# Optimization experiments

Measured on AMD Instinct MI355X. Metric: run time of the kernel, lower is better.

## Reference

```python
import jax, jax.numpy as jnp
import numpy as np

H, W, T = 128, 128, 4
BLOCK_W = 16
N = 1024
CHOL_BOUND = jnp.array([0.5, 0.0, 0.0, 0.5, 0.0, 0.5], dtype=jnp.float32)  # diag lower bound
SCALE = 2.0 * BLOCK_W / W  # gaussian footprint ~ tile-sized in normalized [-1,1] coords


def setup_inputs() -> dict:
    key = jax.random.key(0)
    k1, k2, k3, k4 = jax.random.split(key, 4)
    return {
        "xyz_3D": jax.random.normal(k1, (N, 3), dtype=jnp.float32),
        "cholesky_3D": jax.random.uniform(k2, (N, 6), dtype=jnp.float32),
        "features_dc_3D": jax.random.uniform(k3, (N, 3), dtype=jnp.float32),
        "opacity_3D": jax.random.normal(k4, (N, 1), dtype=jnp.float32),
    }


def _splat(xyz, chol6, feats, opac):
    # activations (match module properties)
    means = jnp.tanh(xyz)                      # [N,3] in [-1,1], (x,y,t)
    c = chol6 + CHOL_BOUND[None, :]            # [N,6]
    alpha_g = jax.nn.sigmoid(opac)             # [N,1]

    # lower-triangular L: rows (x,y,t); layout (0,0)=c0,(1,0)=c1,(2,0)=c2,(1,1)=c3,(2,1)=c4,(2,2)=c5
    zeros = jnp.zeros_like(c[:, 0])
    L = jnp.stack([
        jnp.stack([c[:, 0], zeros,   zeros], -1),
        jnp.stack([c[:, 1], c[:, 3], zeros], -1),
        jnp.stack([c[:, 2], c[:, 4], c[:, 5]], -1),
    ], axis=1) * SCALE                          # [N,3,3]
    Sigma = jnp.einsum('nij,nkj->nik', L, L)    # L L^T, [N,3,3]
    Sinv = jnp.linalg.inv(Sigma)                # [N,3,3]

    # voxel-center grids in normalized [-1,1]
    xs = (jnp.arange(W, dtype=jnp.float32) + 0.5) / W * 2.0 - 1.0
    ys = (jnp.arange(H, dtype=jnp.float32) + 0.5) / H * 2.0 - 1.0
    ts = (jnp.arange(T, dtype=jnp.float32) + 0.5) / T * 2.0 - 1.0

    dx = xs[None, :] - means[:, 0:1]            # [N,W]
    dy = ys[None, :] - means[:, 1:2]            # [N,H]
    dt = ts[None, :] - means[:, 2:3]            # [N,T]

    a  = Sinv[:, 0, 0][:, None, None, None]
    b  = Sinv[:, 1, 1][:, None, None, None]
    cc = Sinv[:, 2, 2][:, None, None, None]
    ab = Sinv[:, 0, 1][:, None, None, None]
    at = Sinv[:, 0, 2][:, None, None, None]
    bt = Sinv[:, 1, 2][:, None, None, None]

    dxw = dx[:, None, None, :]                  # [N,1,1,W]
    dyh = dy[:, None, :, None]                  # [N,1,H,1]
    dtt = dt[:, :, None, None]                  # [N,T,1,1]

    # quadratic form d^T Sigma^{-1} d over the full [N,T,H,W] grid
    q = (a * dxw * dxw + b * dyh * dyh + cc * dtt * dtt
         + 2.0 * ab * dxw * dyh + 2.0 * at * dxw * dtt + 2.0 * bt * dyh * dtt)

    dens = alpha_g[:, :, None, None] * jnp.exp(-0.5 * q)   # [N,T,H,W]
    img = jnp.einsum('nthw,nc->thwc', dens, feats)          # [T,H,W,3]
    return jnp.clip(img, 0.0, 1.0)


def reference(xyz_3D, cholesky_3D, features_dc_3D, opacity_3D):
    return _splat(xyz_3D, cholesky_3D, features_dc_3D, opacity_3D)
```

## Files before the change

kernel.cpp:

```cpp
#include <hip/hip_runtime.h>
#include <hip/hip_fp16.h>


#define GV_H 128
#define GV_W 128
#define GV_T 4
#define GV_NMAX 1024
#define GV_DX 0.015625f
#define K_HALF_LOG2E (-0.72134752044448170f)
#define GV_LOG2E 1.44269504088896340f
#define U_CULL (-20.0f)

typedef float f32x2 __attribute__((ext_vector_type(2)));

__device__ __forceinline__ float fexp2(float x) { return __builtin_amdgcn_exp2f(x); }
__device__ __forceinline__ float frcp(float x)  { return __builtin_amdgcn_rcpf(x); }
__device__ __forceinline__ float flog2(float x) { return __builtin_amdgcn_logf(x); }

__device__ __forceinline__ float fast_tanh(float x) {
    float t = fexp2(2.885390082f * x);
    return fmaf(-2.0f, frcp(t + 1.0f), 1.0f);
}

__global__ __launch_bounds__(1024) void gv_fused_kernel(
    const float* __restrict__ xyz, const float* __restrict__ chol,
    const float* __restrict__ feats, const float* __restrict__ opac,
    float* __restrict__ out, int N)
{
    __shared__ __align__(16) float stab[12800];
    __shared__ int swt[16];

    int b    = blockIdx.x;
    int slab = b & 63;
    int t    = b >> 6;
    int tid  = threadIdx.x;
    int wv   = tid >> 6;
    int lane = tid & 63;

    float y0r = ((float)(slab * 2) + 0.5f) * GV_DX - 1.0f;
    float y1r = y0r + GV_DX;

    float A = 0.f, gy0 = 0.f, gy1 = 0.f, h0 = 0.f, h1 = 0.f, sv = 0.f;
    float rgbits = 0.f, fb = 0.f;
    bool keep = false;

    if (tid < N) {
        int n = tid;
        float mx = fast_tanh(xyz[n * 3 + 0]);
        float my = fast_tanh(xyz[n * 3 + 1]);
        float mt = fast_tanh(xyz[n * 3 + 2]);

        const float sc = 2.0f * 16.0f / (float)GV_W;
        float L00 = sc * (chol[n * 6 + 0] + 0.5f);
        float L10 = sc * (chol[n * 6 + 1]);
        float L20 = sc * (chol[n * 6 + 2]);
        float L11 = sc * (chol[n * 6 + 3] + 0.5f);
        float L21 = sc * (chol[n * 6 + 4]);
        float L22 = sc * (chol[n * 6 + 5] + 0.5f);

        float il0 = frcp(L00), il1 = frcp(L11), il2 = frcp(L22);
        float m10 = -L10 * il0 * il1;
        float m21 = -L21 * il1 * il2;
        float m20 = (L10 * L21 - L11 * L20) * (il0 * il1 * il2);
        float a   = il0 * il0 + m10 * m10 + m20 * m20;
        float sab = m10 * il1 + m20 * m21;
        float sat = m20 * il2;
        float bb  = il1 * il1 + m21 * m21;
        float sbt = m21 * il2;
        float cc  = il2 * il2;
        float ab2 = 2.0f * sab, at2 = 2.0f * sat, bt2 = 2.0f * sbt;

        float o = opac[n];
        float bias = -flog2(1.0f + fexp2(-GV_LOG2E * o));

        float tv = ((float)t + 0.5f) * (2.0f / (float)GV_T) - 1.0f;
        float dt = tv - mt;

        const float k = K_HALF_LOG2E;
        A        = k * a;
        float B  = k * bb;
        float C  = k * ab2;
        float Dx = k * (at2 * dt - 2.0f * a * mx - ab2 * my);
        float Dy = k * (bt2 * dt - 2.0f * bb * my - ab2 * mx);
        float E  = k * (a * mx * mx + bb * my * my + cc * dt * dt
                        + ab2 * mx * my - at2 * mx * dt - bt2 * my * dt) + bias;

        gy0 = fmaf(C, y0r, Dx);
        gy1 = fmaf(C, y1r, Dx);
        h0  = fmaf(fmaf(B, y0r, Dy), y0r, E);
        h1  = fmaf(fmaf(B, y1r, Dy), y1r, E);
        sv  = fexp2(2.0f * A * GV_DX * GV_DX);

        float fr = feats[n * 3 + 0];
        float fg = feats[n * 3 + 1];
        fb       = feats[n * 3 + 2];
        unsigned hr = (unsigned)__half_as_ushort(__float2half_rn(fr))
                    | ((unsigned)__half_as_ushort(__float2half_rn(fg)) << 16);
        rgbits = __uint_as_float(hr);

        float inv2A = 0.5f * frcp(A);
        float xs0 = fminf(fmaxf(-gy0 * inv2A, -1.0f), 1.0f);
        float xs1 = fminf(fmaxf(-gy1 * inv2A, -1.0f), 1.0f);
        float u0  = fmaf(fmaf(A, xs0, gy0), xs0, h0);
        float u1  = fmaf(fmaf(A, xs1, gy1), xs1, h1);
        keep = (fmaxf(u0, u1) > U_CULL);
    }

    unsigned long long bm = __ballot((int)keep);
    int wprefix = __popcll(bm & ((1ull << lane) - 1ull));
    if (lane == 0) swt[wv] = (int)__popcll(bm);
    __syncthreads();

    int base = 0, M = 0;
    #pragma unroll
    for (int k2 = 0; k2 < 16; ++k2) {
        int c = swt[k2];
        if (k2 < wv) base += c;
        M += c;
    }
    if (keep) {
        float4* dst = (float4*)&stab[(base + wprefix) * 8];
        dst[0] = make_float4(A, gy0, gy1, h0);
        dst[1] = make_float4(h1, sv, rgbits, fb);
    }
    __syncthreads();

    int oct  = lane & 15;
    int row  = (lane >> 4) & 1;
    int half = lane >> 5;

    float x0  = ((float)(oct * 8) + 0.5f) * GV_DX - 1.0f;
    float caa = 2.0f * x0 + GV_DX;
    bool  r1  = (row == 1);

    int chunk = (M + 15) >> 4;
    int g0    = wv * chunk;
    int cnt_w = M - g0;
    if (cnt_w > chunk) cnt_w = chunk;
    if (cnt_w < 0) cnt_w = 0;

    f32x2 aR2[8], aG2[8], aB2[8];
    #pragma unroll
    for (int j = 0; j < 8; ++j) {
        aR2[j] = (f32x2)(0.f); aG2[j] = (f32x2)(0.f); aB2[j] = (f32x2)(0.f);
    }

    int i = half;
    #pragma unroll 1
    for (; i + 2 < cnt_w; i += 4) {
        const float4* qa = (const float4*)&stab[(g0 + i) * 8];
        const float4* qb = (const float4*)&stab[(g0 + i + 2) * 8];
        float4 va0 = qa[0], va1 = qa[1];
        float4 vb0 = qb[0], vb1 = qb[1];

        float gya = r1 ? va0.z : va0.y;
        float gyb = r1 ? vb0.z : vb0.y;
        float ha  = r1 ? va1.x : va0.w;
        float hb  = r1 ? vb1.x : vb0.w;

        float ua = fmaf(fmaf(va0.x, x0, gya), x0, ha);
        float ub = fmaf(fmaf(vb0.x, x0, gyb), x0, hb);

        f32x2 e2 = { fexp2(ua), fexp2(ub) };
        f32x2 r2 = { fexp2(GV_DX * fmaf(va0.x, caa, gya)),
                     fexp2(GV_DX * fmaf(vb0.x, caa, gyb)) };
        f32x2 s2 = { va1.y, vb1.y };

        unsigned ba  = __float_as_uint(va1.z);
        unsigned bbb = __float_as_uint(vb1.z);
        f32x2 fr2 = { __half2float(__ushort_as_half((unsigned short)(ba & 0xffffu))),
                      __half2float(__ushort_as_half((unsigned short)(bbb & 0xffffu))) };
        f32x2 fg2 = { __half2float(__ushort_as_half((unsigned short)(ba >> 16))),
                      __half2float(__ushort_as_half((unsigned short)(bbb >> 16))) };
        f32x2 fb2 = { va1.w, vb1.w };

        #pragma unroll
        for (int j = 0; j < 8; ++j) {
            aR2[j] = __builtin_elementwise_fma(e2, fr2, aR2[j]);
            aG2[j] = __builtin_elementwise_fma(e2, fg2, aG2[j]);
            aB2[j] = __builtin_elementwise_fma(e2, fb2, aB2[j]);
            if (j < 7) { e2 *= r2; r2 *= s2; }
        }
    }
    if (i < cnt_w) {
        const float4* qr = (const float4*)&stab[(g0 + i) * 8];
        float4 v0 = qr[0];
        float4 v1 = qr[1];
        float gy = r1 ? v0.z : v0.y;
        float h  = r1 ? v1.x : v0.w;
        float u  = fmaf(fmaf(v0.x, x0, gy), x0, h);
        float e  = fexp2(u);
        float r  = fexp2(GV_DX * fmaf(v0.x, caa, gy));
        float s  = v1.y;
        unsigned bits = __float_as_uint(v1.z);
        float fr = __half2float(__ushort_as_half((unsigned short)(bits & 0xffffu)));
        float fg = __half2float(__ushort_as_half((unsigned short)(bits >> 16)));
        float fbv = v1.w;
        #pragma unroll
        for (int j = 0; j < 8; ++j) {
            aR2[j][0] = fmaf(e, fr,  aR2[j][0]);
            aG2[j][0] = fmaf(e, fg,  aG2[j][0]);
            aB2[j][0] = fmaf(e, fbv, aB2[j][0]);
            if (j < 7) { e *= r; r *= s; }
        }
    }

    float aR[8], aG[8], aB[8];
    #pragma unroll
    for (int j = 0; j < 8; ++j) {
        aR[j] = aR2[j][0] + aR2[j][1];
        aG[j] = aG2[j][0] + aG2[j][1];
        aB[j] = aB2[j][0] + aB2[j][1];
        aR[j] += __shfl_xor(aR[j], 32, 64);
        aG[j] += __shfl_xor(aG[j], 32, 64);
        aB[j] += __shfl_xor(aB[j], 32, 64);
    }

    __syncthreads();

    if (half == 0) {
        float* dst = &stab[(wv * 32 + (row * 16 + oct)) * 25];
        #pragma unroll
        for (int j = 0; j < 8; ++j) {
            dst[j * 3 + 0] = aR[j];
            dst[j * 3 + 1] = aG[j];
            dst[j * 3 + 2] = aB[j];
        }
    }
    __syncthreads();

    if (tid < 2 * GV_W * 3) {
        int o  = tid;
        int c  = o % 3;
        int xr = o / 3;
        int x  = xr & 127;
        int rw = xr >> 7;
        int oc = x >> 3;
        int j  = x & 7;
        int ofs = (rw * 16 + oc) * 25 + j * 3 + c;
        float sacc = 0.f;
        #pragma unroll
        for (int wvI = 0; wvI < 16; ++wvI) sacc += stab[wvI * 800 + ofs];
        int basew = ((t * GV_H + slab * 2) * GV_W) * 3;
        out[basew + o] = fminf(fmaxf(sacc, 0.0f), 1.0f);
    }
}

extern "C" void kernel_launch(void* const* d_in, const int* in_sizes, int n_in,
                              void* d_out, int out_size, void* d_ws, size_t ws_size,
                              hipStream_t stream) {
    const float* xyz   = (const float*)d_in[0];
    const float* chol  = (const float*)d_in[1];
    const float* feats = (const float*)d_in[2];
    const float* opac  = (const float*)d_in[3];
    float* out = (float*)d_out;
    int N = in_sizes[0] / 3;
    if (N > GV_NMAX) N = GV_NMAX;

    int blocks = GV_T * (GV_H / 2);
    gv_fused_kernel<<<blocks, 1024, 0, stream>>>(xyz, chol, feats, opac, out, N);
}
```

Before: 17.13 us.

## Pack both slab rows per lane, interleave gaussians across waves with padding

Each lane now evaluates both output rows of its slab as a packed float2 pair, and lanes are split into four gaussian slots instead of a row/half split. Gaussians are distributed round-robin across waves and slots, with the culled list padded to a multiple of 64 using dummy entries whose exponent is -1e30. This removes the per-wave chunking and the scalar tail loop, and shares the per-gaussian A, s and colour decode across both rows. In exchange it adds a two-step cross-lane shuffle reduction and evaluates the padded dummy gaussians as wasted work.

```diff
diff --git a/kernel.cpp b/kernel.cpp
--- a/kernel.cpp
+++ b/kernel.cpp
@@ -120,24 +120,28 @@
     }
     if (keep) {
         float4* dst = (float4*)&stab[(base + wprefix) * 8];
-        dst[0] = make_float4(A, gy0, gy1, h0);
-        dst[1] = make_float4(h1, sv, rgbits, fb);
+        dst[0] = make_float4(gy0, gy1, h0, h1);
+        dst[1] = make_float4(A, sv, rgbits, fb);
+    }
+    int M64 = (M + 63) & ~63;
+    if (tid >= M && tid < M64) {
+        float4* dst = (float4*)&stab[tid * 8];
+        dst[0] = make_float4(0.f, 0.f, -1e30f, -1e30f);
+        dst[1] = make_float4(0.f, 0.f, 0.f, 0.f);
     }
     __syncthreads();
 
     int oct  = lane & 15;
-    int row  = (lane >> 4) & 1;
-    int half = lane >> 5;
+    int slot = lane >> 4;
 
     float x0  = ((float)(oct * 8) + 0.5f) * GV_DX - 1.0f;
     float caa = 2.0f * x0 + GV_DX;
-    bool  r1  = (row == 1);
-
-    int chunk = (M + 15) >> 4;
-    int g0    = wv * chunk;
-    int cnt_w = M - g0;
-    if (cnt_w > chunk) cnt_w = chunk;
-    if (cnt_w < 0) cnt_w = 0;
+    f32x2 x02  = { x0, x0 };
+    f32x2 caa2 = { caa, caa };
+    f32x2 dx2  = { GV_DX, GV_DX };
+
+    int iters = M64 >> 6;
+    const float* rp = &stab[(wv * 4 + slot) * 8];
 
     f32x2 aR2[8], aG2[8], aB2[8];
     #pragma unroll
@@ -145,34 +149,30 @@
         aR2[j] = (f32x2)(0.f); aG2[j] = (f32x2)(0.f); aB2[j] = (f32x2)(0.f);
     }
 
-    int i = half;
     #pragma unroll 1
-    for (; i + 2 < cnt_w; i += 4) {
-        const float4* qa = (const float4*)&stab[(g0 + i) * 8];
-        const float4* qb = (const float4*)&stab[(g0 + i + 2) * 8];
-        float4 va0 = qa[0], va1 = qa[1];
-        float4 vb0 = qb[0], vb1 = qb[1];
-
-        float gya = r1 ? va0.z : va0.y;
-        float gyb = r1 ? vb0.z : vb0.y;
-        float ha  = r1 ? va1.x : va0.w;
-        float hb  = r1 ? vb1.x : vb0.w;
-
-        float ua = fmaf(fmaf(va0.x, x0, gya), x0, ha);
-        float ub = fmaf(fmaf(vb0.x, x0, gyb), x0, hb);
-
-        f32x2 e2 = { fexp2(ua), fexp2(ub) };
-        f32x2 r2 = { fexp2(GV_DX * fmaf(va0.x, caa, gya)),
-                     fexp2(GV_DX * fmaf(vb0.x, caa, gyb)) };
-        f32x2 s2 = { va1.y, vb1.y };
-
-        unsigned ba  = __float_as_uint(va1.z);
-        unsigned bbb = __float_as_uint(vb1.z);
-        f32x2 fr2 = { __half2float(__ushort_as_half((unsigned short)(ba & 0xffffu))),
-                      __half2float(__ushort_as_half((unsigned short)(bbb & 0xffffu))) };
-        f32x2 fg2 = { __half2float(__ushort_as_half((unsigned short)(ba >> 16))),
-                      __half2float(__ushort_as_half((unsigned short)(bbb >> 16))) };
-        f32x2 fb2 = { va1.w, vb1.w };
+    for (int it = 0; it < iters; ++it) {
+        const float4* q = (const float4*)rp;
+        float4 q0 = q[0];
+        float4 q1 = q[1];
+        rp += 64 * 8;
+
+        f32x2 gy = { q0.x, q0.y };
+        f32x2 hh = { q0.z, q0.w };
+        f32x2 A2 = { q1.x, q1.x };
+
+        f32x2 u2 = __builtin_elementwise_fma(
+                       __builtin_elementwise_fma(A2, x02, gy), x02, hh);
+        f32x2 e2 = { fexp2(u2[0]), fexp2(u2[1]) };
+        f32x2 ra = __builtin_elementwise_fma(A2, caa2, gy) * dx2;
+        f32x2 r2 = { fexp2(ra[0]), fexp2(ra[1]) };
+        f32x2 s2 = { q1.y, q1.y };
+
+        unsigned bits = __float_as_uint(q1.z);
+        float fr = __half2float(__ushort_as_half((unsigned short)(bits & 0xffffu)));
+        float fg = __half2float(__ushort_as_half((unsigned short)(bits >> 16)));
+        f32x2 fr2 = { fr, fr };
+        f32x2 fg2 = { fg, fg };
+        f32x2 fb2 = { q1.w, q1.w };
 
         #pragma unroll
         for (int j = 0; j < 8; ++j) {
@@ -182,65 +182,47 @@
             if (j < 7) { e2 *= r2; r2 *= s2; }
         }
     }
-    if (i < cnt_w) {
-        const float4* qr = (const float4*)&stab[(g0 + i) * 8];
-        float4 v0 = qr[0];
-        float4 v1 = qr[1];
-        float gy = r1 ? v0.z : v0.y;
-        float h  = r1 ? v1.x : v0.w;
-        float u  = fmaf(fmaf(v0.x, x0, gy), x0, h);
-        float e  = fexp2(u);
-        float r  = fexp2(GV_DX * fmaf(v0.x, caa, gy));
-        float s  = v1.y;
-        unsigned bits = __float_as_uint(v1.z);
-        float fr = __half2float(__ushort_as_half((unsigned short)(bits & 0xffffu)));
-        float fg = __half2float(__ushort_as_half((unsigned short)(bits >> 16)));
-        float fbv = v1.w;
+
+    #pragma unroll
+    for (int j = 0; j < 8; ++j) {
+        aR2[j][0] += __shfl_xor(aR2[j][0], 16, 64);
+        aR2[j][1] += __shfl_xor(aR2[j][1], 16, 64);
+        aG2[j][0] += __shfl_xor(aG2[j][0], 16, 64);
+        aG2[j][1] += __shfl_xor(aG2[j][1], 16, 64);
+        aB2[j][0] += __shfl_xor(aB2[j][0], 16, 64);
+        aB2[j][1] += __shfl_xor(aB2[j][1], 16, 64);
+        aR2[j][0] += __shfl_xor(aR2[j][0], 32, 64);
+        aR2[j][1] += __shfl_xor(aR2[j][1], 32, 64);
+        aG2[j][0] += __shfl_xor(aG2[j][0], 32, 64);
+        aG2[j][1] += __shfl_xor(aG2[j][1], 32, 64);
+        aB2[j][0] += __shfl_xor(aB2[j][0], 32, 64);
+        aB2[j][1] += __shfl_xor(aB2[j][1], 32, 64);
+    }
+
+    __syncthreads();
+
+    if (slot == 0) {
+        f32x2* d2 = (f32x2*)&stab[wv * 800];
         #pragma unroll
         for (int j = 0; j < 8; ++j) {
-            aR2[j][0] = fmaf(e, fr,  aR2[j][0]);
-            aG2[j][0] = fmaf(e, fg,  aG2[j][0]);
-            aB2[j][0] = fmaf(e, fbv, aB2[j][0]);
-            if (j < 7) { e *= r; r *= s; }
+            d2[oct * 24 + j * 3 + 0] = aR2[j];
+            d2[oct * 24 + j * 3 + 1] = aG2[j];
+            d2[oct * 24 + j * 3 + 2] = aB2[j];
         }
     }
-
-    float aR[8], aG[8], aB[8];
-    #pragma unroll
-    for (int j = 0; j < 8; ++j) {
-        aR[j] = aR2[j][0] + aR2[j][1];
-        aG[j] = aG2[j][0] + aG2[j][1];
-        aB[j] = aB2[j][0] + aB2[j][1];
-        aR[j] += __shfl_xor(aR[j], 32, 64);
-        aG[j] += __shfl_xor(aG[j], 32, 64);
-        aB[j] += __shfl_xor(aB[j], 32, 64);
-    }
-
-    __syncthreads();
-
-    if (half == 0) {
-        float* dst = &stab[(wv * 32 + (row * 16 + oct)) * 25];
-        #pragma unroll
-        for (int j = 0; j < 8; ++j) {
-            dst[j * 3 + 0] = aR[j];
-            dst[j * 3 + 1] = aG[j];
-            dst[j * 3 + 2] = aB[j];
-        }
-    }
     __syncthreads();
 
     if (tid < 2 * GV_W * 3) {
-        int o  = tid;
-        int c  = o % 3;
-        int xr = o / 3;
-        int x  = xr & 127;
-        int rw = xr >> 7;
-        int oc = x >> 3;
-        int j  = x & 7;
-        int ofs = (rw * 16 + oc) * 25 + j * 3 + c;
+        int o   = tid;
+        int c   = o % 3;
+        int pxr = o / 3;
+        int x   = pxr & 127;
+        int row = pxr >> 7;
+        int op  = x * 3 + c;
         float sacc = 0.f;
         #pragma unroll
-        for (int wvI = 0; wvI < 16; ++wvI) sacc += stab[wvI * 800 + ofs];
+        for (int wvI = 0; wvI < 16; ++wvI)
+            sacc += stab[wvI * 800 + op * 2 + row];
         int basew = ((t * GV_H + slab * 2) * GV_W) * 3;
         out[basew + o] = fminf(fmaxf(sacc, 0.0f), 1.0f);
     }
```

New measurement: 18.23 us. +6.4%, slower.
